# Kernel tuning notes

Measured on AMD Instinct MI355X. Metric: run time of the kernel, lower is better.

## Reference

```python
import jax, jax.numpy as jnp
import numpy as np
from jax import lax

B, T, INPUT, HIDDEN, OUT = 8192, 512, 10, 64, 1


def setup_inputs() -> dict:
    key = jax.random.key(0)
    k1, k2, k3, k4, k5 = jax.random.split(key, 5)
    padded_batch = jax.random.normal(k1, (B, T, INPUT), dtype=jnp.float32)
    lengths = jax.random.randint(k2, (B,), 1, T + 1, dtype=jnp.int64)
    # per-timestep distinct RNN weights, init scale 0.01 as in the torch module
    W_xh = jax.random.normal(k3, (T, INPUT, HIDDEN), dtype=jnp.float32) * 0.01
    W_hh = jax.random.normal(k4, (T, HIDDEN, HIDDEN), dtype=jnp.float32) * 0.01
    W_lin = jax.random.normal(k5, (HIDDEN, OUT), dtype=jnp.float32) * (1.0 / np.sqrt(HIDDEN))
    b_lin = jnp.zeros((OUT,), dtype=jnp.float32)
    return {"padded_batch": padded_batch, "lengths": lengths,
            "W_xh": W_xh, "W_hh": W_hh, "W_lin": W_lin, "b_lin": b_lin}


def reference(padded_batch, lengths, W_xh, W_hh, W_lin, b_lin):
    # padded_batch: [B, T, INPUT]; per-step weights W_xh: [T, INPUT, H], W_hh: [T, H, H]
    Bn = padded_batch.shape[0]
    x_tbd = jnp.swapaxes(padded_batch, 0, 1)  # [T, B, INPUT]
    t_idx = jnp.arange(T)

    def step(h, inputs):
        x_t, wxh, whh, t = inputs
        new_h = jnp.tanh(x_t @ wxh + h @ whh)          # [B, H]
        keep = (t < lengths)[:, None]                   # freeze samples past their length
        h = jnp.where(keep, new_h, h)
        return h, None

    h0 = jnp.zeros((Bn, HIDDEN), dtype=padded_batch.dtype)
    last_hidden, _ = lax.scan(step, h0, (x_tbd, W_xh, W_hh, t_idx))
    return last_hidden @ W_lin + b_lin  # [B, OUT]
```

## Files before the change

### kernel.cpp

```cpp
#include <hip/hip_runtime.h>
#include <stdint.h>

#define T_STEPS 512
#define HID     64
#define INP     10
#define MB      32
#define NTHR    512
#define KS      88
#define HS      72
#define XS      40
#define WT_ELEMS (HID*KS)
#define WT_BYTES (WT_ELEMS*2)
#define WS_SLOTS (WT_BYTES/16)

typedef float  f32x4  __attribute__((ext_vector_type(4)));
typedef short  s16x8  __attribute__((ext_vector_type(8)));
typedef __bf16 bf16x8 __attribute__((ext_vector_type(8)));

typedef const __attribute__((address_space(1))) unsigned int* gp_t;
typedef __attribute__((address_space(3))) unsigned int*       lp_t;

__device__ __forceinline__ short f2bf(float f) {
    unsigned u = __builtin_bit_cast(unsigned, f);
    u = (u + 0x7FFFu + ((u >> 16) & 1u)) >> 16;
    return (short)u;
}
__device__ __forceinline__ short f2bfh(float f) {
    return __builtin_bit_cast(short, (__bf16)f);
}
__device__ __forceinline__ float bf2f(short s) {
    unsigned u = ((unsigned)(unsigned short)s) << 16;
    return __builtin_bit_cast(float, u);
}

__global__ __launch_bounds__(256) void prep_w(const float* __restrict__ Wxh,
                                              const float* __restrict__ Whh,
                                              short* __restrict__ Wc) {
    __shared__ float s_hh[64 * 65];
    __shared__ float s_xh[INP * 65];
    const int t = blockIdx.x, tid = threadIdx.x;
    for (int i = tid; i < 64 * 64; i += 256)
        s_hh[(i >> 6) * 65 + (i & 63)] = Whh[t * 4096 + i];
    for (int i = tid; i < INP * 64; i += 256)
        s_xh[(i >> 6) * 65 + (i & 63)] = Wxh[t * (INP * 64) + i];
    __syncthreads();
    short* dst = Wc + (size_t)t * WT_ELEMS;
    for (int i = tid; i < WT_ELEMS; i += 256) {
        const int n = i / KS, k = i % KS;
        float v = 0.f;
        if (k < 64)      v = s_hh[k * 65 + n];
        else if (k < 74) v = s_xh[(k - 64) * 65 + n];
        dst[i] = f2bf(v);
    }
}

__global__ __launch_bounds__(NTHR, 2) void rnn_main(const float* __restrict__ X,
                                                    const int* __restrict__ L,
                                                    const short* __restrict__ Wc,
                                                    const float* __restrict__ Wlin,
                                                    const float* __restrict__ blin,
                                                    float* __restrict__ out) {
    __shared__ __attribute__((aligned(16))) short Wb[2][WT_ELEMS + 16];
    __shared__ __attribute__((aligned(16))) short hb[2][MB * HS];
    __shared__ __attribute__((aligned(16))) short xb[2][MB * XS];
    __shared__ int len_s[MB];

    const int tid  = threadIdx.x;
    const int lane = tid & 63;
    const int w    = tid >> 6;
    const int mt   = w >> 2;
    const int nt   = w & 3;
    const int q    = lane >> 4;
    const int l    = lane & 15;
    const long long bbase = (long long)blockIdx.x * MB;

    auto issue_w = [&](int tp) {
        const char* src = (const char*)Wc + (size_t)tp * WT_BYTES;
        char* dst = (char*)&Wb[tp & 1][0];
        __builtin_amdgcn_global_load_lds((gp_t)(src + tid * 16),
                                         (lp_t)(dst + tid * 16), 16, 0, 0);
        if (tid < WS_SLOTS - 512)
            __builtin_amdgcn_global_load_lds((gp_t)(src + (tid + 512) * 16),
                                             (lp_t)(dst + (tid + 512) * 16), 16, 0, 0);
    };

    const int xs = tid / INP, xi = tid - (tid / INP) * INP;

    if (tid < MB) len_s[tid] = L[bbase + tid];
    for (int i = tid; i < MB * HS; i += NTHR) hb[0][i] = 0;
    for (int i = tid; i < MB * XS; i += NTHR) { xb[0][i] = 0; xb[1][i] = 0; }
    if (tid < 16) { Wb[0][WT_ELEMS + tid] = 0; Wb[1][WT_ELEMS + tid] = 0; }
    issue_w(0);
    __syncthreads();

    float xrA = 0.f, xrB = 0.f;
    if (tid < MB * INP) {
        xb[0][xs * XS + xi] = f2bfh(X[(bbase + xs) * (T_STEPS * INP) + 0 * INP + xi]);
        xrA = X[(bbase + xs) * (T_STEPS * INP) + 1 * INP + xi];
    }
    __syncthreads();

    float hc[4] = {0.f, 0.f, 0.f, 0.f};
    int len4[4];
#pragma unroll
    for (int r = 0; r < 4; ++r) len4[r] = len_s[mt * 16 + q * 4 + r];
    const int colw = nt * 16 + l;
    const int woff = colw * KS + q * 8;
    const int arow = mt * 16 + l;

    auto stepf = [&](int t, float& xr_held, float& xr_new) {
        const int cur = t & 1, nxt = cur ^ 1;

        if (tid < MB * INP && t + 2 < T_STEPS)
            xr_new = X[(bbase + xs) * (T_STEPS * INP) + (long long)(t + 2) * INP + xi];
        if (t + 1 < T_STEPS) issue_w(t + 1);
        if (tid < MB * INP) xb[nxt][xs * XS + xi] = f2bfh(xr_held);

        const s16x8 a0 = *(const s16x8*)&hb[cur][arow * HS + q * 8];
        const s16x8 a1 = *(const s16x8*)&hb[cur][arow * HS + 32 + q * 8];
        const s16x8 a2 = *(const s16x8*)&xb[cur][arow * XS + q * 8];
        const s16x8 b0 = *(const s16x8*)&Wb[cur][woff];
        const s16x8 b1 = *(const s16x8*)&Wb[cur][woff + 32];
        const s16x8 b2 = *(const s16x8*)&Wb[cur][woff + 64];

        f32x4 z = {0.f, 0.f, 0.f, 0.f};
        f32x4 acc0 = __builtin_amdgcn_mfma_f32_16x16x32_bf16(
                  __builtin_bit_cast(bf16x8, a0), __builtin_bit_cast(bf16x8, b0), z, 0, 0, 0);
        f32x4 acc1 = __builtin_amdgcn_mfma_f32_16x16x32_bf16(
                  __builtin_bit_cast(bf16x8, a1), __builtin_bit_cast(bf16x8, b1), z, 0, 0, 0);
        f32x4 acc2 = __builtin_amdgcn_mfma_f32_16x16x32_bf16(
                  __builtin_bit_cast(bf16x8, a2), __builtin_bit_cast(bf16x8, b2), z, 0, 0, 0);

#pragma unroll
        for (int r = 0; r < 4; ++r) {
            const float a  = acc0[r] + acc1[r] + acc2[r];
            const float e  = __expf(2.f * a);
            const float th = 1.f - 2.f * __builtin_amdgcn_rcpf(e + 1.f);
            hc[r] = (t < len4[r]) ? th : hc[r];
            hb[nxt][(mt * 16 + q * 4 + r) * HS + colw] = f2bfh(hc[r]);
        }
        __syncthreads();
    };

    for (int tt = 0; tt < T_STEPS; tt += 2) {
        stepf(tt,     xrA, xrB);
        stepf(tt + 1, xrB, xrA);
    }

    const float wl = Wlin[lane];
    const float bl = blin[0];
#pragma unroll
    for (int it = 0; it < 4; ++it) {
        const int s = w + it * 8;
        float v = bf2f(hb[0][s * HS + lane]) * wl;
#pragma unroll
        for (int off = 32; off > 0; off >>= 1) v += __shfl_down(v, off);
        if (lane == 0) out[bbase + s] = v + bl;
    }
}

extern "C" void kernel_launch(void* const* d_in, const int* in_sizes, int n_in,
                              void* d_out, int out_size, void* d_ws, size_t ws_size,
                              hipStream_t stream) {
    const float* X    = (const float*)d_in[0];
    const int*   L    = (const int*)d_in[1];
    const float* Wxh  = (const float*)d_in[2];
    const float* Whh  = (const float*)d_in[3];
    const float* Wlin = (const float*)d_in[4];
    const float* blin = (const float*)d_in[5];
    float*       out  = (float*)d_out;
    short*       Wc   = (short*)d_ws;

    prep_w<<<T_STEPS, 256, 0, stream>>>(Wxh, Whh, Wc);
    rnn_main<<<8192 / MB, NTHR, 0, stream>>>(X, L, Wc, Wlin, blin, out);
}
```

Measured before the change: 537.2 us.

## Restructure RNN kernel into per-wave recurrence with 8-slot async weight/input ring

Shrinks the block to two waves, each owning 16 samples and computing all 64 hidden columns. This removes the per-step block-wide barrier that previously gated the hidden-state exchange between eight waves. Weights and raw fp32 inputs are streamed into an 8-slot LDS ring with a lookahead of 6 steps using direct global-to-LDS loads. A barrier with a vmcnt wait runs every two steps. The trade-off is fewer waves per block, more MFMA work per wave, and a more intricate wait-count scheme whose correctness depends on the exact number of outstanding loads.

```diff
diff --git a/kernel.cpp b/kernel.cpp
--- a/kernel.cpp
+++ b/kernel.cpp
@@ -4,14 +4,17 @@
 #define T_STEPS 512
 #define HID     64
 #define INP     10
-#define MB      32
-#define NTHR    512
 #define KS      88
 #define HS      72
-#define XS      40
 #define WT_ELEMS (HID*KS)
 #define WT_BYTES (WT_ELEMS*2)
 #define WS_SLOTS (WT_BYTES/16)
+
+#define LOOK   6
+#define RING   8
+#define WSLOTP 768
+#define WR_SH  (WSLOTP*8)
+#define XR_DW  384
 
 typedef float  f32x4  __attribute__((ext_vector_type(4)));
 typedef short  s16x8  __attribute__((ext_vector_type(8)));
@@ -54,109 +57,144 @@
     }
 }
 
-__global__ __launch_bounds__(NTHR, 2) void rnn_main(const float* __restrict__ X,
-                                                    const int* __restrict__ L,
-                                                    const short* __restrict__ Wc,
-                                                    const float* __restrict__ Wlin,
-                                                    const float* __restrict__ blin,
-                                                    float* __restrict__ out) {
-    __shared__ __attribute__((aligned(16))) short Wb[2][WT_ELEMS + 16];
-    __shared__ __attribute__((aligned(16))) short hb[2][MB * HS];
-    __shared__ __attribute__((aligned(16))) short xb[2][MB * XS];
-    __shared__ int len_s[MB];
+__global__ __launch_bounds__(128) void rnn_main(const float* __restrict__ X,
+                                                const int* __restrict__ L,
+                                                const short* __restrict__ Wc,
+                                                const float* __restrict__ Wlin,
+                                                const float* __restrict__ blin,
+                                                float* __restrict__ out) {
+    __shared__ __attribute__((aligned(16))) short Wr[RING][WR_SH];
+    __shared__ __attribute__((aligned(16))) float Xr[RING][XR_DW];
+    __shared__ __attribute__((aligned(16))) short hbuf[2][16 * HS];
+    __shared__ int len_s[32];
 
     const int tid  = threadIdx.x;
     const int lane = tid & 63;
     const int w    = tid >> 6;
-    const int mt   = w >> 2;
-    const int nt   = w & 3;
     const int q    = lane >> 4;
     const int l    = lane & 15;
-    const long long bbase = (long long)blockIdx.x * MB;
-
-    auto issue_w = [&](int tp) {
-        const char* src = (const char*)Wc + (size_t)tp * WT_BYTES;
-        char* dst = (char*)&Wb[tp & 1][0];
-        __builtin_amdgcn_global_load_lds((gp_t)(src + tid * 16),
-                                         (lp_t)(dst + tid * 16), 16, 0, 0);
-        if (tid < WS_SLOTS - 512)
-            __builtin_amdgcn_global_load_lds((gp_t)(src + (tid + 512) * 16),
-                                             (lp_t)(dst + (tid + 512) * 16), 16, 0, 0);
+    const long long sb = (long long)blockIdx.x * 32 + w * 16;
+
+    int voffW[6];
+#pragma unroll
+    for (int i = 0; i < 6; ++i) {
+        int s = w * 384 + i * 64 + lane;
+        if (s > WS_SLOTS - 1) s = WS_SLOTS - 1;
+        voffW[i] = s * 16;
+    }
+    int voffX[3];
+#pragma unroll
+    for (int i = 0; i < 3; ++i) {
+        int d = i * 64 + lane;
+        if (d > 159) d = 159;
+        const int s = d / 10, e = d - 10 * s;
+        voffX[i] = s * (T_STEPS * INP * 4) + e * 4;
+    }
+    const char* xbase = (const char*)X + (size_t)sb * (T_STEPS * INP * 4);
+
+    if (lane < 16) len_s[w * 16 + lane] = L[sb + lane];
+    for (int i = lane; i < 16 * HS; i += 64) hbuf[w][i] = 0;
+    int len4[4];
+#pragma unroll
+    for (int r = 0; r < 4; ++r) len4[r] = len_s[w * 16 + q * 4 + r];
+
+    auto issue_x = [&](int tw, int slot) {
+        const char* src = xbase + (size_t)tw * (INP * 4);
+        char* dst = (char*)&Xr[slot][w * 192];
+#pragma unroll
+        for (int i = 0; i < 3; ++i)
+            __builtin_amdgcn_global_load_lds((gp_t)(src + voffX[i]),
+                                             (lp_t)(dst + i * 256), 4, 0, 0);
     };
-
-    const int xs = tid / INP, xi = tid - (tid / INP) * INP;
-
-    if (tid < MB) len_s[tid] = L[bbase + tid];
-    for (int i = tid; i < MB * HS; i += NTHR) hb[0][i] = 0;
-    for (int i = tid; i < MB * XS; i += NTHR) { xb[0][i] = 0; xb[1][i] = 0; }
-    if (tid < 16) { Wb[0][WT_ELEMS + tid] = 0; Wb[1][WT_ELEMS + tid] = 0; }
-    issue_w(0);
-    __syncthreads();
-
-    float xrA = 0.f, xrB = 0.f;
-    if (tid < MB * INP) {
-        xb[0][xs * XS + xi] = f2bfh(X[(bbase + xs) * (T_STEPS * INP) + 0 * INP + xi]);
-        xrA = X[(bbase + xs) * (T_STEPS * INP) + 1 * INP + xi];
-    }
-    __syncthreads();
-
-    float hc[4] = {0.f, 0.f, 0.f, 0.f};
-    int len4[4];
-#pragma unroll
-    for (int r = 0; r < 4; ++r) len4[r] = len_s[mt * 16 + q * 4 + r];
-    const int colw = nt * 16 + l;
-    const int woff = colw * KS + q * 8;
-    const int arow = mt * 16 + l;
-
-    auto stepf = [&](int t, float& xr_held, float& xr_new) {
-        const int cur = t & 1, nxt = cur ^ 1;
-
-        if (tid < MB * INP && t + 2 < T_STEPS)
-            xr_new = X[(bbase + xs) * (T_STEPS * INP) + (long long)(t + 2) * INP + xi];
-        if (t + 1 < T_STEPS) issue_w(t + 1);
-        if (tid < MB * INP) xb[nxt][xs * XS + xi] = f2bfh(xr_held);
-
-        const s16x8 a0 = *(const s16x8*)&hb[cur][arow * HS + q * 8];
-        const s16x8 a1 = *(const s16x8*)&hb[cur][arow * HS + 32 + q * 8];
-        const s16x8 a2 = *(const s16x8*)&xb[cur][arow * XS + q * 8];
-        const s16x8 b0 = *(const s16x8*)&Wb[cur][woff];
-        const s16x8 b1 = *(const s16x8*)&Wb[cur][woff + 32];
-        const s16x8 b2 = *(const s16x8*)&Wb[cur][woff + 64];
-
-        f32x4 z = {0.f, 0.f, 0.f, 0.f};
-        f32x4 acc0 = __builtin_amdgcn_mfma_f32_16x16x32_bf16(
-                  __builtin_bit_cast(bf16x8, a0), __builtin_bit_cast(bf16x8, b0), z, 0, 0, 0);
-        f32x4 acc1 = __builtin_amdgcn_mfma_f32_16x16x32_bf16(
-                  __builtin_bit_cast(bf16x8, a1), __builtin_bit_cast(bf16x8, b1), z, 0, 0, 0);
-        f32x4 acc2 = __builtin_amdgcn_mfma_f32_16x16x32_bf16(
-                  __builtin_bit_cast(bf16x8, a2), __builtin_bit_cast(bf16x8, b2), z, 0, 0, 0);
-
-#pragma unroll
-        for (int r = 0; r < 4; ++r) {
-            const float a  = acc0[r] + acc1[r] + acc2[r];
-            const float e  = __expf(2.f * a);
-            const float th = 1.f - 2.f * __builtin_amdgcn_rcpf(e + 1.f);
-            hc[r] = (t < len4[r]) ? th : hc[r];
-            hb[nxt][(mt * 16 + q * 4 + r) * HS + colw] = f2bfh(hc[r]);
+    auto issue_w = [&](int tw, int slot) {
+        const char* src = (const char*)Wc + (size_t)tw * WT_BYTES;
+        char* dst = (char*)&Wr[slot][0] + w * 6144;
+#pragma unroll
+        for (int i = 0; i < 6; ++i)
+            __builtin_amdgcn_global_load_lds((gp_t)(src + voffW[i]),
+                                             (lp_t)(dst + i * 1024), 16, 0, 0);
+    };
+
+#pragma unroll
+    for (int k = 0; k < LOOK; ++k) { issue_x(k, k); issue_w(k, k); }
+
+    float hc[4][4];
+#pragma unroll
+    for (int nt = 0; nt < 4; ++nt)
+#pragma unroll
+        for (int r = 0; r < 4; ++r) hc[nt][r] = 0.f;
+
+    const short* hrow = &hbuf[w][l * HS];
+
+    for (int it = 0; it < T_STEPS / 8; ++it) {
+#pragma unroll
+        for (int k = 0; k < 8; ++k) {
+            const int t = it * 8 + k;
+
+            if ((k & 1) == 0) {
+                asm volatile("s_waitcnt vmcnt(36)" ::: "memory");
+                __builtin_amdgcn_s_barrier();
+            }
+
+            const int tw = (t + LOOK < T_STEPS) ? (t + LOOK) : (T_STEPS - 1);
+            issue_x(tw, (k + LOOK) & 7);
+            issue_w(tw, (k + LOOK) & 7);
+
+            s16x8 bf[4][3];
+#pragma unroll
+            for (int nt = 0; nt < 4; ++nt)
+#pragma unroll
+                for (int c = 0; c < 3; ++c)
+                    bf[nt][c] = *(const s16x8*)&Wr[k][(nt * 16 + l) * KS + c * 32 + q * 8];
+
+            const s16x8 a0 = *(const s16x8*)(hrow + q * 8);
+            const s16x8 a1 = *(const s16x8*)(hrow + 32 + q * 8);
+            const float2* xp = (const float2*)&Xr[k][w * 192 + l * 10 + q * 8];
+            const float2 p0 = xp[0], p1 = xp[1], p2 = xp[2], p3 = xp[3];
+            const float xv[8] = {p0.x, p0.y, p1.x, p1.y, p2.x, p2.y, p3.x, p3.y};
+            s16x8 a2;
+#pragma unroll
+            for (int j = 0; j < 8; ++j)
+                a2[j] = (q * 8 + j < INP) ? f2bfh(xv[j]) : (short)0;
+
+            f32x4 acc[4];
+#pragma unroll
+            for (int nt = 0; nt < 4; ++nt) {
+                f32x4 z = {0.f, 0.f, 0.f, 0.f};
+                acc[nt] = __builtin_amdgcn_mfma_f32_16x16x32_bf16(
+                    __builtin_bit_cast(bf16x8, a0), __builtin_bit_cast(bf16x8, bf[nt][0]), z, 0, 0, 0);
+                acc[nt] = __builtin_amdgcn_mfma_f32_16x16x32_bf16(
+                    __builtin_bit_cast(bf16x8, a1), __builtin_bit_cast(bf16x8, bf[nt][1]), acc[nt], 0, 0, 0);
+                acc[nt] = __builtin_amdgcn_mfma_f32_16x16x32_bf16(
+                    __builtin_bit_cast(bf16x8, a2), __builtin_bit_cast(bf16x8, bf[nt][2]), acc[nt], 0, 0, 0);
+            }
+
+#pragma unroll
+            for (int nt = 0; nt < 4; ++nt)
+#pragma unroll
+                for (int r = 0; r < 4; ++r) {
+                    const float a  = acc[nt][r];
+                    const float e  = __expf(2.f * a);
+                    const float th = 1.f - 2.f * __builtin_amdgcn_rcpf(e + 1.f);
+                    hc[nt][r] = (t < len4[r]) ? th : hc[nt][r];
+                    hbuf[w][(q * 4 + r) * HS + nt * 16 + l] = f2bfh(hc[nt][r]);
+                }
         }
-        __syncthreads();
-    };
-
-    for (int tt = 0; tt < T_STEPS; tt += 2) {
-        stepf(tt,     xrA, xrB);
-        stepf(tt + 1, xrB, xrA);
-    }
-
-    const float wl = Wlin[lane];
-    const float bl = blin[0];
-#pragma unroll
-    for (int it = 0; it < 4; ++it) {
-        const int s = w + it * 8;
-        float v = bf2f(hb[0][s * HS + lane]) * wl;
-#pragma unroll
-        for (int off = 32; off > 0; off >>= 1) v += __shfl_down(v, off);
-        if (lane == 0) out[bbase + s] = v + bl;
-    }
+    }
+
+    asm volatile("s_waitcnt vmcnt(0)" ::: "memory");
+
+    const s16x8 h0 = *(const s16x8*)&hbuf[w][l * HS + q * 16];
+    const s16x8 h1 = *(const s16x8*)&hbuf[w][l * HS + q * 16 + 8];
+    float v = 0.f;
+#pragma unroll
+    for (int j = 0; j < 8; ++j) {
+        v += bf2f(h0[j]) * Wlin[q * 16 + j];
+        v += bf2f(h1[j]) * Wlin[q * 16 + 8 + j];
+    }
+    v += __shfl_xor(v, 16);
+    v += __shfl_xor(v, 32);
+    if (q == 0) out[sb + l] = v + blin[0];
 }
 
 extern "C" void kernel_launch(void* const* d_in, const int* in_sizes, int n_in,
@@ -172,5 +210,5 @@
     short*       Wc   = (short*)d_ws;
 
     prep_w<<<T_STEPS, 256, 0, stream>>>(Wxh, Whh, Wc);
-    rnn_main<<<8192 / MB, NTHR, 0, stream>>>(X, L, Wc, Wlin, blin, out);
-}
+    rnn_main<<<8192 / 32, 128, 0, stream>>>(X, L, Wc, Wlin, blin, out);
+}
```

New measurement: 864.6 us. +60.9%, slower.
